# Performance work log

Hardware: AMD Instinct MI355X
Metric: run time of the kernel (lower is better)

The kernel has to match this reference:

```python
import jax, jax.numpy as jnp
import numpy as np

D_IN = 1024
D_OUT = 1024

def setup_inputs() -> dict:
    key = jax.random.key(0)
    kx, kq, kk, kv = jax.random.split(key, 4)
    x = jax.random.normal(kx, (4, 2048, D_IN), dtype=jnp.float32)
    # torch Linear weights are [d_out, d_in]; store as [d_in, d_out] for x @ W
    s = 1.0 / np.sqrt(D_IN)
    Wq = jax.random.uniform(kq, (D_IN, D_OUT), jnp.float32, -s, s)
    Wk = jax.random.uniform(kk, (D_IN, D_OUT), jnp.float32, -s, s)
    Wv = jax.random.uniform(kv, (D_IN, D_OUT), jnp.float32, -s, s)
    return {"x": x, "Wq": Wq, "Wk": Wk, "Wv": Wv}

def reference(x, Wq, Wk, Wv):
    # x: [b, n, d_in]
    n = x.shape[1]
    q = jnp.einsum('bnd,de->bne', x, Wq)
    k = jnp.einsum('bnd,de->bne', x, Wk)
    v = jnp.einsum('bnd,de->bne', x, Wv)
    scores = jnp.einsum('bqe,bke->bqk', q, k)  # [b, n, n]
    causal = jnp.tril(jnp.ones((n, n), dtype=bool))  # True = keep
    scores = jnp.where(causal, scores, -jnp.inf)
    attn = jax.nn.softmax(scores / jnp.sqrt(jnp.float32(k.shape[-1])), axis=-1)
    # dropout p=0.0 -> identity
    return jnp.einsum('bqk,bke->bqe', attn, v)
```

## Files before the change

### kernel.cpp

```cpp
#include <hip/hip_runtime.h>
#include <hip/hip_bf16.h>
#include <stdint.h>

#define D_ 1024
#define NSEQ 2048

typedef __attribute__((ext_vector_type(8))) short bf16x8;
typedef __attribute__((ext_vector_type(4))) float f32x4;

static __device__ __forceinline__ unsigned short f2bf(float x) {
    union { __hip_bfloat16 h; unsigned short u; } cv;
    cv.h = __float2bfloat16(x);
    return cv.u;
}

static __device__ __forceinline__ void gload_lds16(const void* g, void* l) {
    __builtin_amdgcn_global_load_lds(
        (const __attribute__((address_space(1))) unsigned int*)(uintptr_t)g,
        (__attribute__((address_space(3))) unsigned int*)(uintptr_t)l, 16, 0, 0);
}

__global__ __launch_bounds__(256) void cvt_x(const float* __restrict__ x,
                                             __hip_bfloat16* __restrict__ xb) {
    int i = blockIdx.x * 256 + threadIdx.x;
    float4 v = reinterpret_cast<const float4*>(x)[i];
    ushort4 o;
    o.x = f2bf(v.x); o.y = f2bf(v.y); o.z = f2bf(v.z); o.w = f2bf(v.w);
    reinterpret_cast<ushort4*>(xb)[i] = o;
}

__global__ __launch_bounds__(256) void wt_kernel(const float* __restrict__ Wq,
                                                 const float* __restrict__ Wk,
                                                 const float* __restrict__ Wv,
                                                 __hip_bfloat16* __restrict__ Wt) {
    const float* W = (blockIdx.z == 0) ? Wq : (blockIdx.z == 1) ? Wk : Wv;
    unsigned short* O = (unsigned short*)(Wt + (size_t)blockIdx.z * D_ * D_);
    __shared__ float tile[32][33];
    int r0 = blockIdx.y * 32, c0 = blockIdx.x * 32;
    int t = threadIdx.x;
    int r = t >> 3, c4 = (t & 7) * 4;
    float4 v = *reinterpret_cast<const float4*>(&W[(size_t)(r0 + r) * D_ + c0 + c4]);
    tile[r][c4 + 0] = v.x; tile[r][c4 + 1] = v.y;
    tile[r][c4 + 2] = v.z; tile[r][c4 + 3] = v.w;
    __syncthreads();
    int er = t >> 3, dc = (t & 7) * 4;
    ushort4 pk;
    pk.x = f2bf(tile[dc + 0][er]); pk.y = f2bf(tile[dc + 1][er]);
    pk.z = f2bf(tile[dc + 2][er]); pk.w = f2bf(tile[dc + 3][er]);
    *reinterpret_cast<ushort4*>(&O[(size_t)(c0 + er) * D_ + r0 + dc]) = pk;
}

__global__ __launch_bounds__(512, 2) void gemm_qkv(
    const __hip_bfloat16* __restrict__ A,
    const __hip_bfloat16* __restrict__ Bt,
    void* __restrict__ q_out, void* __restrict__ k_out, void* __restrict__ vt_out) {
    constexpr int NT = 16;
    extern __shared__ char lds[];

    const int m0 = blockIdx.x * 256, n0 = blockIdx.y * 128;
    const int tid = threadIdx.x, lane = tid & 63, wid = tid >> 6;
    const int wm = wid >> 1, wn = wid & 1;
    const int lr = lane & 15, lk = lane >> 4;

    const __hip_bfloat16* Apan = A + (size_t)m0 * 1024;
    const __hip_bfloat16* Bpan = Bt + (size_t)n0 * 1024;

    const __hip_bfloat16* asrc[4];
    const __hip_bfloat16* bsrc[2];
#pragma unroll
    for (int r = 0; r < 4; ++r) {
        const int c = (wid * 4 + r) * 64 + lane;
        const int row = c >> 3, slot = c & 7;
        asrc[r] = Apan + (size_t)row * 1024 + (slot ^ (row & 7)) * 8;
    }
#pragma unroll
    for (int r = 0; r < 2; ++r) {
        const int c = (wid * 2 + r) * 64 + lane;
        const int row = c >> 3, slot = c & 7;
        bsrc[r] = Bpan + (size_t)row * 1024 + (slot ^ (row & 7)) * 8;
    }

    auto stage = [&](int s) {
        char* base = lds + (s % 3) * 49152;
#pragma unroll
        for (int r = 0; r < 4; ++r) {
            gload_lds16(asrc[r], base + (wid * 4 + r) * 1024);
            asrc[r] += 64;
        }
#pragma unroll
        for (int r = 0; r < 2; ++r) {
            gload_lds16(bsrc[r], base + 32768 + (wid * 2 + r) * 1024);
            bsrc[r] += 64;
        }
    };

    const int sw = lr & 7;
    const int slot0 = (lk ^ sw) * 16, slot1 = ((4 + lk) ^ sw) * 16;

    f32x4 acc[4][4] = {};

    stage(0); stage(1);

    for (int t = 0; t < NT; ++t) {
        if (t >= NT - 1) asm volatile("s_waitcnt vmcnt(0)" ::: "memory");
        else             asm volatile("s_waitcnt vmcnt(6)" ::: "memory");
        __builtin_amdgcn_s_barrier();
        if (t + 2 < NT) stage(t + 2);

        const char* Ab = lds + (t % 3) * 49152;
        const char* Bb = Ab + 32768;
        bf16x8 af0[4], af1[4], bf0[4], bf1[4];
#pragma unroll
        for (int m = 0; m < 4; ++m) {
            const int ra = (wm * 64 + m * 16 + lr) * 128;
            const int rb = (wn * 64 + m * 16 + lr) * 128;
            af0[m] = *reinterpret_cast<const bf16x8*>(Ab + ra + slot0);
            af1[m] = *reinterpret_cast<const bf16x8*>(Ab + ra + slot1);
            bf0[m] = *reinterpret_cast<const bf16x8*>(Bb + rb + slot0);
            bf1[m] = *reinterpret_cast<const bf16x8*>(Bb + rb + slot1);
        }
        __builtin_amdgcn_s_setprio(1);
#pragma unroll
        for (int m = 0; m < 4; ++m)
#pragma unroll
            for (int n = 0; n < 4; ++n)
                acc[m][n] = __builtin_amdgcn_mfma_f32_16x16x32_bf16(af0[m], bf0[n], acc[m][n], 0, 0, 0);
#pragma unroll
        for (int m = 0; m < 4; ++m)
#pragma unroll
            for (int n = 0; n < 4; ++n)
                acc[m][n] = __builtin_amdgcn_mfma_f32_16x16x32_bf16(af1[m], bf1[n], acc[m][n], 0, 0, 0);
        __builtin_amdgcn_s_setprio(0);
    }

#pragma unroll
    for (int m = 0; m < 4; ++m)
#pragma unroll
        for (int n = 0; n < 4; ++n) {
            const int rbase = m0 + wm * 64 + m * 16 + lk * 4;
            const int cbase = n0 + wn * 64 + n * 16 + lr;
            const int seg = cbase >> 10, e = cbase & 1023;
            if (seg < 2) {
                unsigned short* C = (unsigned short*)(seg == 0 ? q_out : k_out);
#pragma unroll
                for (int j = 0; j < 4; ++j)
                    C[(size_t)(rbase + j) * D_ + e] = f2bf(acc[m][n][j]);
            } else {
                unsigned short* Vt = (unsigned short*)vt_out;
                const int b = rbase >> 11, nq = rbase & 2047;
                ushort4 pk;
                pk.x = f2bf(acc[m][n][0]); pk.y = f2bf(acc[m][n][1]);
                pk.z = f2bf(acc[m][n][2]); pk.w = f2bf(acc[m][n][3]);
                *reinterpret_cast<ushort4*>(&Vt[(((size_t)b << 10) + e) * NSEQ + nq]) = pk;
            }
        }
}

template <int MODE>
__global__ __launch_bounds__(256) void gemm128(const __hip_bfloat16* __restrict__ A, int lda,
                                               const __hip_bfloat16* __restrict__ Bt, int ldb,
                                               void* __restrict__ o0, void* __restrict__ o1,
                                               const float* __restrict__ rinv) {
    int bx, by, bz;
    if (MODE == 2) {
        const int fid = blockIdx.x;
        bz = fid & 3;
        const int t = fid >> 2;
        bx = (int)((sqrtf(8.0f * t + 1.0f) - 1.0f) * 0.5f);
        while ((bx + 1) * (bx + 2) / 2 <= t) ++bx;
        while (bx * (bx + 1) / 2 > t) --bx;
        by = t - bx * (bx + 1) / 2;
    } else {
        const int fid = blockIdx.x;
        const int bxr = fid & 15;
        bx = (fid & 256) ? 15 - bxr : bxr;
        bz = (fid >> 4) & 3;
        by = fid >> 6;
    }

    const __hip_bfloat16* Ab = A;
    const __hip_bfloat16* Bb = Bt;
    int Kdim = 1024;
    if (MODE == 2) { Ab += (size_t)bz * NSEQ * lda; Bb += (size_t)bz * NSEQ * ldb; }
    if (MODE == 3) { Ab += (size_t)bz * NSEQ * lda; Bb += (size_t)bz * D_ * ldb; Kdim = (bx + 1) * 128; }

    const int m0 = bx * 128, n0 = by * 128;

    __shared__ __hip_bfloat16 As[128 * 64];
    __shared__ __hip_bfloat16 Bs[128 * 64];

    const int tid = threadIdx.x;
    const int lane = tid & 63, wid = tid >> 6;
    const int wm = wid >> 1, wn = wid & 1;
    const int lr = lane & 15, lk = lane >> 4;

    const __hip_bfloat16* asrc[4];
    const __hip_bfloat16* bsrc[4];
#pragma unroll
    for (int r = 0; r < 4; ++r) {
        const int chunk = r * 256 + tid;
        const int row = chunk >> 3, slot = chunk & 7;
        const int col = ((slot ^ (row & 7)) * 8);
        asrc[r] = Ab + (size_t)(m0 + row) * lda + col;
        bsrc[r] = Bb + (size_t)(n0 + row) * ldb + col;
    }

    const int sw = lr & 7;
    const int slotA0 = (lk ^ sw) * 16, slotA1 = ((4 + lk) ^ sw) * 16;

    f32x4 acc[4][4] = {};

    for (int k0 = 0; k0 < Kdim; k0 += 64) {
#pragma unroll
        for (int r = 0; r < 4; ++r) {
            gload_lds16(asrc[r], (char*)As + r * 4096 + wid * 1024);
            gload_lds16(bsrc[r], (char*)Bs + r * 4096 + wid * 1024);
            asrc[r] += 64; bsrc[r] += 64;
        }
        __syncthreads();

        bf16x8 af0[4], bf0[4], af1[4], bf1[4];
#pragma unroll
        for (int m = 0; m < 4; ++m) {
            const int ra = (wm * 64 + m * 16 + lr) * 128;
            const int rb = (wn * 64 + m * 16 + lr) * 128;
            af0[m] = *reinterpret_cast<const bf16x8*>((const char*)As + ra + slotA0);
            af1[m] = *reinterpret_cast<const bf16x8*>((const char*)As + ra + slotA1);
            bf0[m] = *reinterpret_cast<const bf16x8*>((const char*)Bs + rb + slotA0);
            bf1[m] = *reinterpret_cast<const bf16x8*>((const char*)Bs + rb + slotA1);
        }
#pragma unroll
        for (int m = 0; m < 4; ++m)
#pragma unroll
            for (int n = 0; n < 4; ++n)
                acc[m][n] = __builtin_amdgcn_mfma_f32_16x16x32_bf16(af0[m], bf0[n], acc[m][n], 0, 0, 0);
#pragma unroll
        for (int m = 0; m < 4; ++m)
#pragma unroll
            for (int n = 0; n < 4; ++n)
                acc[m][n] = __builtin_amdgcn_mfma_f32_16x16x32_bf16(af1[m], bf1[n], acc[m][n], 0, 0, 0);
        __syncthreads();
    }

    if (MODE == 2) {
        unsigned short* P = (unsigned short*)o0 + (size_t)bz * NSEQ * NSEQ;
#pragma unroll
        for (int m = 0; m < 4; ++m)
#pragma unroll
            for (int n = 0; n < 4; ++n) {
                const int rbase = m0 + wm * 64 + m * 16 + lk * 4;
                const int cbase = n0 + wn * 64 + n * 16 + lr;
#pragma unroll
                for (int j = 0; j < 4; ++j) {
                    float p = (cbase > rbase + j) ? 0.0f
                              : __expf(acc[m][n][j] * 0.03125f);
                    acc[m][n][j] = p;
                    P[(size_t)(rbase + j) * NSEQ + cbase] = f2bf(p);
                }
            }
        float* Pl = (float*)o1;
        const int pcol = by * 2 + wn;
#pragma unroll
        for (int m = 0; m < 4; ++m)
#pragma unroll
            for (int j = 0; j < 4; ++j) {
                float sm = (acc[m][0][j] + acc[m][1][j]) + (acc[m][2][j] + acc[m][3][j]);
#pragma unroll
                for (int w = 1; w < 16; w <<= 1) sm += __shfl_xor(sm, w, 64);
                if (lr == 0) {
                    const int row = bz * NSEQ + m0 + wm * 64 + m * 16 + lk * 4 + j;
                    Pl[row * 32 + pcol] = sm;
                }
            }
    } else {
        float* O = (float*)o0 + (size_t)bz * NSEQ * D_;
#pragma unroll
        for (int m = 0; m < 4; ++m)
#pragma unroll
            for (int n = 0; n < 4; ++n) {
                const int rbase = m0 + wm * 64 + m * 16 + lk * 4;
                const int cbase = n0 + wn * 64 + n * 16 + lr;
#pragma unroll
                for (int j = 0; j < 4; ++j)
                    O[(size_t)(rbase + j) * D_ + cbase] =
                        acc[m][n][j] * rinv[bz * NSEQ + rbase + j];
            }
    }
}

__global__ __launch_bounds__(256) void sum_merge(const float* __restrict__ Pl,
                                                 float* __restrict__ rinv) {
    int row = blockIdx.x * 256 + threadIdx.x;
    int q = row & 2047;
    int nc = 2 * ((q >> 7) + 1);
    float l = 0.f;
    for (int c = 0; c < nc; ++c) l += Pl[row * 32 + c];
    rinv[row] = 1.0f / l;
}

extern "C" void kernel_launch(void* const* d_in, const int* in_sizes, int n_in,
                              void* d_out, int out_size, void* d_ws, size_t ws_size,
                              hipStream_t stream) {
    const float* x  = (const float*)d_in[0];
    const float* Wq = (const float*)d_in[1];
    const float* Wk = (const float*)d_in[2];
    const float* Wv = (const float*)d_in[3];

    char* ws = (char*)d_ws;
    unsigned short* P    = (unsigned short*)(ws);
    __hip_bfloat16* Xb   = (__hip_bfloat16*)(ws + 67108864);
    __hip_bfloat16* Q    = (__hip_bfloat16*)(ws + 83886080);
    __hip_bfloat16* K    = (__hip_bfloat16*)(ws + 100663296);
    __hip_bfloat16* Vt   = (__hip_bfloat16*)(ws + 117440512);
    __hip_bfloat16* Wt   = (__hip_bfloat16*)(ws + 134217728);
    float*  Pl = (float*)(ws + 67108864);
    float*  rl = (float*)(ws + 69206016);

    cvt_x<<<8192, 256, 0, stream>>>(x, Xb);
    wt_kernel<<<dim3(32, 32, 3), 256, 0, stream>>>(Wq, Wk, Wv, Wt);

    gemm_qkv<<<dim3(32, 24), 512, 147456, stream>>>(Xb, Wt, Q, K, Vt);

    gemm128<2><<<dim3(544), 256, 0, stream>>>(Q, 1024, K, 1024, P, Pl, nullptr);
    sum_merge<<<32, 256, 0, stream>>>(Pl, rl);
    gemm128<3><<<dim3(512), 256, 0, stream>>>((const __hip_bfloat16*)P, 2048, Vt, 2048,
                                              d_out, nullptr, rl);
}
```

Before: 163.7 us.

## Merge input prep kernels and replace triple-buffered QKV GEMM with single-buffer sync loop

Fuses the x conversion and weight transpose kernels into a single prep launch, which removes one kernel launch. It also rewrites the QKV GEMM mainloop: the 3-stage async LDS pipeline with vmcnt waits becomes a single static LDS buffer loaded and consumed each iteration between two __syncthreads. The smaller LDS footprint (48KB instead of 144KB) may allow more blocks per CU. The trade-off is that global-to-LDS load latency is no longer hidden behind MFMA work.

```diff
diff --git a/kernel.cpp b/kernel.cpp
--- a/kernel.cpp
+++ b/kernel.cpp
@@ -20,24 +20,29 @@
         (__attribute__((address_space(3))) unsigned int*)(uintptr_t)l, 16, 0, 0);
 }
 
-__global__ __launch_bounds__(256) void cvt_x(const float* __restrict__ x,
-                                             __hip_bfloat16* __restrict__ xb) {
-    int i = blockIdx.x * 256 + threadIdx.x;
-    float4 v = reinterpret_cast<const float4*>(x)[i];
-    ushort4 o;
-    o.x = f2bf(v.x); o.y = f2bf(v.y); o.z = f2bf(v.z); o.w = f2bf(v.w);
-    reinterpret_cast<ushort4*>(xb)[i] = o;
-}
-
-__global__ __launch_bounds__(256) void wt_kernel(const float* __restrict__ Wq,
-                                                 const float* __restrict__ Wk,
-                                                 const float* __restrict__ Wv,
-                                                 __hip_bfloat16* __restrict__ Wt) {
-    const float* W = (blockIdx.z == 0) ? Wq : (blockIdx.z == 1) ? Wk : Wv;
-    unsigned short* O = (unsigned short*)(Wt + (size_t)blockIdx.z * D_ * D_);
+__global__ __launch_bounds__(256) void prep(const float* __restrict__ x,
+                                            const float* __restrict__ Wq,
+                                            const float* __restrict__ Wk,
+                                            const float* __restrict__ Wv,
+                                            __hip_bfloat16* __restrict__ xb,
+                                            __hip_bfloat16* __restrict__ Wt) {
     __shared__ float tile[32][33];
-    int r0 = blockIdx.y * 32, c0 = blockIdx.x * 32;
-    int t = threadIdx.x;
+    const int b = blockIdx.x;
+    const int t = threadIdx.x;
+    if (b < 8192) {
+        int i = b * 256 + t;
+        float4 v = reinterpret_cast<const float4*>(x)[i];
+        ushort4 o;
+        o.x = f2bf(v.x); o.y = f2bf(v.y); o.z = f2bf(v.z); o.w = f2bf(v.w);
+        reinterpret_cast<ushort4*>(xb)[i] = o;
+        return;
+    }
+    const int b2 = b - 8192;
+    const int z = b2 >> 10, rem = b2 & 1023;
+    const int cx = rem & 31, cy = rem >> 5;
+    const float* W = (z == 0) ? Wq : (z == 1) ? Wk : Wv;
+    unsigned short* O = (unsigned short*)(Wt + (size_t)z * D_ * D_);
+    int r0 = cy * 32, c0 = cx * 32;
     int r = t >> 3, c4 = (t & 7) * 4;
     float4 v = *reinterpret_cast<const float4*>(&W[(size_t)(r0 + r) * D_ + c0 + c4]);
     tile[r][c4 + 0] = v.x; tile[r][c4 + 1] = v.y;
@@ -50,12 +55,14 @@
     *reinterpret_cast<ushort4*>(&O[(size_t)(c0 + er) * D_ + r0 + dc]) = pk;
 }
 
-__global__ __launch_bounds__(512, 2) void gemm_qkv(
+__global__ __launch_bounds__(512) void gemm_qkv(
     const __hip_bfloat16* __restrict__ A,
     const __hip_bfloat16* __restrict__ Bt,
     void* __restrict__ q_out, void* __restrict__ k_out, void* __restrict__ vt_out) {
     constexpr int NT = 16;
-    extern __shared__ char lds[];
+
+    __shared__ __hip_bfloat16 As[256 * 64];
+    __shared__ __hip_bfloat16 Bs[128 * 64];
 
     const int m0 = blockIdx.x * 256, n0 = blockIdx.y * 128;
     const int tid = threadIdx.x, lane = tid & 63, wid = tid >> 6;
@@ -80,44 +87,33 @@
         bsrc[r] = Bpan + (size_t)row * 1024 + (slot ^ (row & 7)) * 8;
     }
 
-    auto stage = [&](int s) {
-        char* base = lds + (s % 3) * 49152;
-#pragma unroll
-        for (int r = 0; r < 4; ++r) {
-            gload_lds16(asrc[r], base + (wid * 4 + r) * 1024);
-            asrc[r] += 64;
-        }
-#pragma unroll
-        for (int r = 0; r < 2; ++r) {
-            gload_lds16(bsrc[r], base + 32768 + (wid * 2 + r) * 1024);
-            bsrc[r] += 64;
-        }
-    };
-
     const int sw = lr & 7;
     const int slot0 = (lk ^ sw) * 16, slot1 = ((4 + lk) ^ sw) * 16;
 
     f32x4 acc[4][4] = {};
 
-    stage(0); stage(1);
-
     for (int t = 0; t < NT; ++t) {
-        if (t >= NT - 1) asm volatile("s_waitcnt vmcnt(0)" ::: "memory");
-        else             asm volatile("s_waitcnt vmcnt(6)" ::: "memory");
-        __builtin_amdgcn_s_barrier();
-        if (t + 2 < NT) stage(t + 2);
-
-        const char* Ab = lds + (t % 3) * 49152;
-        const char* Bb = Ab + 32768;
+#pragma unroll
+        for (int r = 0; r < 4; ++r) {
+            gload_lds16(asrc[r], (char*)As + (wid * 4 + r) * 1024);
+            asrc[r] += 64;
+        }
+#pragma unroll
+        for (int r = 0; r < 2; ++r) {
+            gload_lds16(bsrc[r], (char*)Bs + (wid * 2 + r) * 1024);
+            bsrc[r] += 64;
+        }
+        __syncthreads();
+
         bf16x8 af0[4], af1[4], bf0[4], bf1[4];
 #pragma unroll
         for (int m = 0; m < 4; ++m) {
             const int ra = (wm * 64 + m * 16 + lr) * 128;
             const int rb = (wn * 64 + m * 16 + lr) * 128;
-            af0[m] = *reinterpret_cast<const bf16x8*>(Ab + ra + slot0);
-            af1[m] = *reinterpret_cast<const bf16x8*>(Ab + ra + slot1);
-            bf0[m] = *reinterpret_cast<const bf16x8*>(Bb + rb + slot0);
-            bf1[m] = *reinterpret_cast<const bf16x8*>(Bb + rb + slot1);
+            af0[m] = *reinterpret_cast<const bf16x8*>((const char*)As + ra + slot0);
+            af1[m] = *reinterpret_cast<const bf16x8*>((const char*)As + ra + slot1);
+            bf0[m] = *reinterpret_cast<const bf16x8*>((const char*)Bs + rb + slot0);
+            bf1[m] = *reinterpret_cast<const bf16x8*>((const char*)Bs + rb + slot1);
         }
         __builtin_amdgcn_s_setprio(1);
 #pragma unroll
@@ -131,6 +127,7 @@
             for (int n = 0; n < 4; ++n)
                 acc[m][n] = __builtin_amdgcn_mfma_f32_16x16x32_bf16(af1[m], bf1[n], acc[m][n], 0, 0, 0);
         __builtin_amdgcn_s_setprio(0);
+        __syncthreads();
     }
 
 #pragma unroll
@@ -316,10 +313,9 @@
     float*  Pl = (float*)(ws + 67108864);
     float*  rl = (float*)(ws + 69206016);
 
-    cvt_x<<<8192, 256, 0, stream>>>(x, Xb);
-    wt_kernel<<<dim3(32, 32, 3), 256, 0, stream>>>(Wq, Wk, Wv, Wt);
-
-    gemm_qkv<<<dim3(32, 24), 512, 147456, stream>>>(Xb, Wt, Q, K, Vt);
+    prep<<<11264, 256, 0, stream>>>(x, Wq, Wk, Wv, Xb, Wt);
+
+    gemm_qkv<<<dim3(32, 24), 512, 0, stream>>>(Xb, Wt, Q, K, Vt);
 
     gemm128<2><<<dim3(544), 256, 0, stream>>>(Q, 1024, K, 1024, P, Pl, nullptr);
     sum_merge<<<32, 256, 0, stream>>>(Pl, rl);
```

New measurement: 177.1 us. 8.2% more time.
